# Optimization experiments

Measured on AMD Instinct MI355X. Metric: run time of the kernel, lower is better.

Reference implementation:

```python
import jax, jax.numpy as jnp
import numpy as np


def setup_inputs() -> dict:
    key = jax.random.key(0)
    x = jax.random.normal(key, (2, 2, 128, 256, 256), dtype=jnp.float32)
    return {"x": x}


def reference(x):
    # NonMaximaSuppression3d with kernel_size=(3,3,3): a voxel survives iff it is
    # strictly greater than all 26 neighbors; border voxels are always suppressed.
    sl = {-1: slice(0, -2), 0: slice(1, -1), 1: slice(2, None)}
    center = x[..., 1:-1, 1:-1, 1:-1]  # [B, CH, D-2, H-2, W-2]
    m = jnp.ones(center.shape, dtype=bool)
    for dd in (-1, 0, 1):
        for dh in (-1, 0, 1):
            for dw in (-1, 0, 1):
                if dd == 0 and dh == 0 and dw == 0:
                    continue
                m = m & (center > x[..., sl[dd], sl[dh], sl[dw]])
    mask = jnp.zeros(x.shape, dtype=bool).at[..., 1:-1, 1:-1, 1:-1].set(m)
    return x * mask.astype(x.dtype)
```

## Files before the change

### kernel.cpp

```cpp
#include <hip/hip_runtime.h>


#define W 256
#define H 256
#define D 128
#define PLANE (H * W)
#define VOL (D * PLANE)
#define CH 32
#define WAVES 8

__device__ __forceinline__ float max3f(float a, float b, float c) {
    return fmaxf(fmaxf(a, b), c);
}

struct PState {
    float pm[4];
    float pc[4];
    float c[4];
};

__device__ __forceinline__ void plane_state(const float* __restrict__ base, PState& s) {
    float4 t = *reinterpret_cast<const float4*>(base - W);
    float4 m = *reinterpret_cast<const float4*>(base);
    float4 b = *reinterpret_cast<const float4*>(base + W);
    float tl = __shfl_up(t.w, 1), tr = __shfl_down(t.x, 1);
    float ml = __shfl_up(m.w, 1), mr = __shfl_down(m.x, 1);
    float bl = __shfl_up(b.w, 1), br = __shfl_down(b.x, 1);

    float rt[4], rb[4], rm[4], nc[4];
    rt[0] = max3f(tl, t.x, t.y); rt[1] = max3f(t.x, t.y, t.z);
    rt[2] = max3f(t.y, t.z, t.w); rt[3] = max3f(t.z, t.w, tr);
    rb[0] = max3f(bl, b.x, b.y); rb[1] = max3f(b.x, b.y, b.z);
    rb[2] = max3f(b.y, b.z, b.w); rb[3] = max3f(b.z, b.w, br);
    rm[0] = max3f(ml, m.x, m.y); rm[1] = max3f(m.x, m.y, m.z);
    rm[2] = max3f(m.y, m.z, m.w); rm[3] = max3f(m.z, m.w, mr);
    nc[0] = fmaxf(ml, m.y); nc[1] = fmaxf(m.x, m.z);
    nc[2] = fmaxf(m.y, m.w); nc[3] = fmaxf(m.z, mr);

    s.c[0] = m.x; s.c[1] = m.y; s.c[2] = m.z; s.c[3] = m.w;
    #pragma unroll
    for (int j = 0; j < 4; ++j) {
        s.pm[j] = max3f(rt[j], rm[j], rb[j]);
        s.pc[j] = max3f(rt[j], nc[j], rb[j]);
    }
}

__global__ __launch_bounds__(WAVES * 64) void nms3d_kernel(const float* __restrict__ x,
                                                           float* __restrict__ out) {
    const int lane = threadIdx.x & 63;
    const int wv = threadIdx.x >> 6;
    const int HG = H / WAVES;
    const int hgroup = blockIdx.x % HG;
    const int bc = (blockIdx.x / HG) & 3;
    const int dchunk = blockIdx.x / (HG * 4);
    const int h = hgroup * WAVES + wv;
    const int w0 = lane * 4;
    const int dlo = dchunk * CH;
    const int dhi = dlo + CH;
    const int rowoff = bc * VOL + h * W + w0;

    const float4 zero4 = make_float4(0.f, 0.f, 0.f, 0.f);

    if (h == 0 || h == H - 1) {
        for (int d = dlo; d < dhi; ++d)
            *reinterpret_cast<float4*>(out + rowoff + d * PLANE) = zero4;
        return;
    }

    if (dlo == 0)
        *reinterpret_cast<float4*>(out + rowoff) = zero4;
    if (dhi == D)
        *reinterpret_cast<float4*>(out + rowoff + (D - 1) * PLANE) = zero4;

    const int dstart = (dlo == 0) ? 1 : dlo;
    const int dend = (dhi == D) ? D - 1 : dhi;

    float pm0[4];
    PState s1;
    {
        PState tmp;
        plane_state(x + rowoff + (dstart - 1) * PLANE, tmp);
        #pragma unroll
        for (int j = 0; j < 4; ++j) pm0[j] = tmp.pm[j];
        plane_state(x + rowoff + dstart * PLANE, s1);
    }

    const bool vj0 = (lane != 0);
    const bool vj3 = (lane != 63);

    #pragma unroll 4
    for (int d = dstart; d < dend; ++d) {
        PState s2;
        plane_state(x + rowoff + (d + 1) * PLANE, s2);

        float4 o;
        {
            float nb0 = max3f(pm0[0], s1.pc[0], s2.pm[0]);
            float nb1 = max3f(pm0[1], s1.pc[1], s2.pm[1]);
            float nb2 = max3f(pm0[2], s1.pc[2], s2.pm[2]);
            float nb3 = max3f(pm0[3], s1.pc[3], s2.pm[3]);
            o.x = (vj0 && s1.c[0] > nb0) ? s1.c[0] : 0.f;
            o.y = (s1.c[1] > nb1) ? s1.c[1] : 0.f;
            o.z = (s1.c[2] > nb2) ? s1.c[2] : 0.f;
            o.w = (vj3 && s1.c[3] > nb3) ? s1.c[3] : 0.f;
        }
        *reinterpret_cast<float4*>(out + rowoff + d * PLANE) = o;

        #pragma unroll
        for (int j = 0; j < 4; ++j) {
            pm0[j] = s1.pm[j];
            s1.pm[j] = s2.pm[j];
            s1.pc[j] = s2.pc[j];
            s1.c[j] = s2.c[j];
        }
    }
}

extern "C" void kernel_launch(void* const* d_in, const int* in_sizes, int n_in,
                              void* d_out, int out_size, void* d_ws, size_t ws_size,
                              hipStream_t stream) {
    const float* x = (const float*)d_in[0];
    float* out = (float*)d_out;

    const int HG = H / WAVES;
    const int blocks = (D / CH) * 4 * HG;
    hipLaunchKernelGGL(nms3d_kernel, dim3(blocks), dim3(WAVES * 64), 0, stream,
                       x, out);
}
```

Measured before the change: 49.89 us.

## Remap blocks per XCD, halve depth chunk, use nontemporal output stores

After: 46.58 us, median of 2. 6.6% less time.

```diff
diff --git a/kernel.cpp b/kernel.cpp
--- a/kernel.cpp
+++ b/kernel.cpp
@@ -6,8 +6,11 @@
 #define D 128
 #define PLANE (H * W)
 #define VOL (D * PLANE)
-#define CH 32
+#define CH 16
 #define WAVES 8
+#define NXCD 8
+
+typedef float v4f __attribute__((ext_vector_type(4)));
 
 __device__ __forceinline__ float max3f(float a, float b, float c) {
     return fmaxf(fmaxf(a, b), c);
@@ -45,32 +48,40 @@
     }
 }
 
+__device__ __forceinline__ void nt_store4(float* p, float a, float b, float c, float d) {
+    v4f v = {a, b, c, d};
+    __builtin_nontemporal_store(v, reinterpret_cast<v4f*>(p));
+}
+
 __global__ __launch_bounds__(WAVES * 64) void nms3d_kernel(const float* __restrict__ x,
                                                            float* __restrict__ out) {
     const int lane = threadIdx.x & 63;
     const int wv = threadIdx.x >> 6;
     const int HG = H / WAVES;
-    const int hgroup = blockIdx.x % HG;
-    const int bc = (blockIdx.x / HG) & 3;
-    const int dchunk = blockIdx.x / (HG * 4);
+    const int NWG = (D / CH) * 4 * HG;
+    const int CPX = NWG / NXCD;
+
+    const int lb = (blockIdx.x % NXCD) * CPX + blockIdx.x / NXCD;
+
+    const int hgroup = lb % HG;
+    const int bc = (lb / HG) & 3;
+    const int dchunk = lb / (HG * 4);
     const int h = hgroup * WAVES + wv;
     const int w0 = lane * 4;
     const int dlo = dchunk * CH;
     const int dhi = dlo + CH;
     const int rowoff = bc * VOL + h * W + w0;
 
-    const float4 zero4 = make_float4(0.f, 0.f, 0.f, 0.f);
-
     if (h == 0 || h == H - 1) {
         for (int d = dlo; d < dhi; ++d)
-            *reinterpret_cast<float4*>(out + rowoff + d * PLANE) = zero4;
+            nt_store4(out + rowoff + d * PLANE, 0.f, 0.f, 0.f, 0.f);
         return;
     }
 
     if (dlo == 0)
-        *reinterpret_cast<float4*>(out + rowoff) = zero4;
+        nt_store4(out + rowoff, 0.f, 0.f, 0.f, 0.f);
     if (dhi == D)
-        *reinterpret_cast<float4*>(out + rowoff + (D - 1) * PLANE) = zero4;
+        nt_store4(out + rowoff + (D - 1) * PLANE, 0.f, 0.f, 0.f, 0.f);
 
     const int dstart = (dlo == 0) ? 1 : dlo;
     const int dend = (dhi == D) ? D - 1 : dhi;
@@ -93,18 +104,15 @@
         PState s2;
         plane_state(x + rowoff + (d + 1) * PLANE, s2);
 
-        float4 o;
-        {
-            float nb0 = max3f(pm0[0], s1.pc[0], s2.pm[0]);
-            float nb1 = max3f(pm0[1], s1.pc[1], s2.pm[1]);
-            float nb2 = max3f(pm0[2], s1.pc[2], s2.pm[2]);
-            float nb3 = max3f(pm0[3], s1.pc[3], s2.pm[3]);
-            o.x = (vj0 && s1.c[0] > nb0) ? s1.c[0] : 0.f;
-            o.y = (s1.c[1] > nb1) ? s1.c[1] : 0.f;
-            o.z = (s1.c[2] > nb2) ? s1.c[2] : 0.f;
-            o.w = (vj3 && s1.c[3] > nb3) ? s1.c[3] : 0.f;
-        }
-        *reinterpret_cast<float4*>(out + rowoff + d * PLANE) = o;
+        float nb0 = max3f(pm0[0], s1.pc[0], s2.pm[0]);
+        float nb1 = max3f(pm0[1], s1.pc[1], s2.pm[1]);
+        float nb2 = max3f(pm0[2], s1.pc[2], s2.pm[2]);
+        float nb3 = max3f(pm0[3], s1.pc[3], s2.pm[3]);
+        nt_store4(out + rowoff + d * PLANE,
+                  (vj0 && s1.c[0] > nb0) ? s1.c[0] : 0.f,
+                  (s1.c[1] > nb1) ? s1.c[1] : 0.f,
+                  (s1.c[2] > nb2) ? s1.c[2] : 0.f,
+                  (vj3 && s1.c[3] > nb3) ? s1.c[3] : 0.f);
 
         #pragma unroll
         for (int j = 0; j < 4; ++j) {
```
